# Kernel optimization log

Hardware: AMD Instinct MI355X
Metric: run time of the kernel (lower is better)

## Reference

```python
import jax, jax.numpy as jnp
import numpy as np

MAX_SET_SIZE = 32  # f1_query_max_set_size


def setup_inputs() -> dict:
    key = jax.random.key(0)
    k1, k2, k3, k4 = jax.random.split(key, 4)
    B, Lq, L, d_qk, d_v = 8, 512, 4096, 64, 64
    q = jax.random.normal(k1, (B, Lq, d_qk), dtype=jnp.float32)
    k = jax.random.normal(k2, (B, L, d_qk), dtype=jnp.float32)
    v = jax.random.normal(k3, (B, L, d_v), dtype=jnp.float32)
    mask = jax.random.randint(k4, (B * Lq, L), 0, 2).astype(bool)
    return {"q": q, "k": k, "v": v, "mask": mask}


def _query_conditioned_subset_pool(rank_scores, v, batch_idx, mask, max_set_size):
    # rank_scores/mask: [N, L]; v: [B, L, d_v]
    N, L = rank_scores.shape
    keep = min(max_set_size, L)
    neg_inf = jnp.finfo(rank_scores.dtype).min
    masked_scores = jnp.where(mask, rank_scores.astype(jnp.float32), neg_inf)
    _, top_idx = jax.lax.top_k(masked_scores, keep)          # [N, keep]
    picked = jnp.take_along_axis(mask, top_idx, axis=1)
    sortable = jnp.where(picked, top_idx, L)                 # sentinel L for unpicked
    sortable = jnp.sort(sortable, axis=1)                    # restore index order
    picked = sortable < L
    safe_idx = jnp.where(picked, sortable, 0)                # [N, keep]
    sel_v = v[batch_idx[:, None], safe_idx]                  # [N, keep, d_v]
    sel_scores = jnp.take_along_axis(rank_scores, safe_idx, axis=1)
    sel_scores = jnp.where(picked, sel_scores, neg_inf)
    attn = jax.nn.softmax(sel_scores, axis=1)
    non_empty = picked.any(axis=1, keepdims=True)
    attn = jnp.where(picked & non_empty, attn, jnp.zeros_like(attn))
    return jnp.einsum('nk,nkd->nd', attn.astype(sel_v.dtype), sel_v)


def reference(q, k, v, mask):
    B, Lq, d_qk = q.shape
    L = k.shape[1]
    d_v = v.shape[-1]
    scale = 1.0 / float(np.sqrt(d_qk))
    # rank_scores [B, Lq, L] -> flat chains [B*Lq, L]
    rank_scores = jnp.einsum('bqd,bld->bql', q, k) * scale
    rs_flat = rank_scores.reshape(B * Lq, L)
    batch_idx = jnp.repeat(jnp.arange(B), Lq)
    # f1 = mean over masked support: sum_v / clamp(count, 1)
    mask_f = mask.astype(q.dtype)                            # [B*Lq, L]
    count = jnp.clip(mask_f.sum(axis=1), 1.0, None)          # [B*Lq]
    sum_v = jnp.einsum('bql,bld->bqd', mask_f.reshape(B, Lq, L), v).reshape(B * Lq, d_v)
    mean_out = sum_v / count[:, None]
    # f1_query_mode='add': query-conditioned restricted pooling over top-k subset
    q_ctx = _query_conditioned_subset_pool(rs_flat, v, batch_idx, mask, MAX_SET_SIZE)
    out = mean_out + q_ctx
    return out.reshape(B, Lq, d_v)
```

## Files before the change

### kernel.cpp

```cpp
#include <hip/hip_runtime.h>
#include <float.h>
#include <math.h>

#define LQ   512
#define LL   4096
#define DD   64
#define KEEP 32
#define NB   8
#define NROWS (NB * LQ)

#define RT    32
#define NLC   8
#define LC    (LL / NLC)
#define LSP   128
#define NPAIR (LC / LSP)

#define WS_CI    (NROWS * NLC * KEEP)
#define WS_VT    (2 * NROWS * NLC * KEEP)
#define WS_TOTAL (WS_VT + (NB * DD * LL) / 2)

#define MASKED_KEY 0x00800000u

typedef short  bf16x8 __attribute__((ext_vector_type(8)));
typedef float  f32x4  __attribute__((ext_vector_type(4)));

__device__ __forceinline__ float dot4(float4 a, float4 b) {
    return a.x * b.x + a.y * b.y + a.z * b.z + a.w * b.w;
}
__device__ __forceinline__ unsigned short f2bf(float f) {
    unsigned int u = __float_as_uint(f);
    return (unsigned short)((u + 0x7FFFu + ((u >> 16) & 1u)) >> 16);
}
__device__ __forceinline__ unsigned int f2key(float f) {
    unsigned int u = __float_as_uint(f);
    return ((int)u < 0) ? ~u : (u | 0x80000000u);
}

#define TP_LB 256
__global__ __launch_bounds__(256) void k_vt(
    const float* __restrict__ v, unsigned short* __restrict__ vt)
{
    __shared__ unsigned short tile[DD][TP_LB + 8];
    const int t  = threadIdx.x;
    const int b  = blockIdx.x >> 4;
    const int l0 = (blockIdx.x & 15) * TP_LB;

    const float4* vg = reinterpret_cast<const float4*>(v + ((size_t)b * LL + l0) * DD);
    #pragma unroll
    for (int i = 0; i < 16; ++i) {
        int j = t + 256 * i;
        float4 f = vg[j];
        int l = j >> 4, dq = (j & 15) * 4;
        tile[dq + 0][l] = f2bf(f.x);
        tile[dq + 1][l] = f2bf(f.y);
        tile[dq + 2][l] = f2bf(f.z);
        tile[dq + 3][l] = f2bf(f.w);
    }
    __syncthreads();
    const int d = t >> 2, seg = t & 3;
    const uint4* src = reinterpret_cast<const uint4*>(&tile[d][seg * 64]);
    uint4* dst = reinterpret_cast<uint4*>(vt + ((size_t)b * DD + d) * LL + l0 + seg * 64);
    #pragma unroll
    for (int i = 0; i < 8; ++i) dst[i] = src[i];
}

__global__ __launch_bounds__(256) void k_mean(
    const int* __restrict__ mask,
    const unsigned short* __restrict__ vt,
    float* __restrict__ out)
{
    __shared__ float sums[4][4][16][16];
    __shared__ float cnt_s[4][16];

    const int t     = threadIdx.x;
    const int wave  = t >> 6;
    const int lane  = t & 63;
    const int n0    = blockIdx.x * 16;
    const int b     = n0 / LQ;
    const int row_a = lane & 15;
    const int chunk = lane >> 4;

    const int* mrow = mask + (size_t)(n0 + row_a) * LL + wave * 1024 + chunk * 8;
    const unsigned short* vbase = vt + (size_t)b * DD * LL + wave * 1024 + chunk * 8;

    f32x4 acc[4];
    #pragma unroll
    for (int dt = 0; dt < 4; ++dt) acc[dt] = (f32x4){0.f, 0.f, 0.f, 0.f};
    int cnt = 0;

    for (int l0 = 0; l0 < 1024; l0 += 32) {
        int4 ma = *reinterpret_cast<const int4*>(mrow + l0);
        int4 mb = *reinterpret_cast<const int4*>(mrow + l0 + 4);
        cnt += (ma.x != 0) + (ma.y != 0) + (ma.z != 0) + (ma.w != 0)
             + (mb.x != 0) + (mb.y != 0) + (mb.z != 0) + (mb.w != 0);
        unsigned int p[4];
        p[0] = (ma.x ? 0x3F80u : 0u) | (ma.y ? 0x3F800000u : 0u);
        p[1] = (ma.z ? 0x3F80u : 0u) | (ma.w ? 0x3F800000u : 0u);
        p[2] = (mb.x ? 0x3F80u : 0u) | (mb.y ? 0x3F800000u : 0u);
        p[3] = (mb.z ? 0x3F80u : 0u) | (mb.w ? 0x3F800000u : 0u);
        bf16x8 afrag = *reinterpret_cast<bf16x8*>(p);
        #pragma unroll
        for (int dt = 0; dt < 4; ++dt) {
            bf16x8 bfrag = *reinterpret_cast<const bf16x8*>(
                vbase + (size_t)(dt * 16 + row_a) * LL + l0);
            acc[dt] = __builtin_amdgcn_mfma_f32_16x16x32_bf16(afrag, bfrag, acc[dt], 0, 0, 0);
        }
    }
    cnt += __shfl_xor(cnt, 16);
    cnt += __shfl_xor(cnt, 32);
    if (lane < 16) cnt_s[wave][lane] = (float)cnt;
    #pragma unroll
    for (int dt = 0; dt < 4; ++dt)
        #pragma unroll
        for (int r = 0; r < 4; ++r)
            sums[wave][dt][chunk * 4 + r][row_a] = acc[dt][r];
    __syncthreads();

    const int d = t & 63, rgrp = t >> 6;
    #pragma unroll
    for (int rr = 0; rr < 4; ++rr) {
        const int row = rgrp * 4 + rr;
        float s = sums[0][d >> 4][row][d & 15] + sums[1][d >> 4][row][d & 15]
                + sums[2][d >> 4][row][d & 15] + sums[3][d >> 4][row][d & 15];
        float c = cnt_s[0][row] + cnt_s[1][row] + cnt_s[2][row] + cnt_s[3][row];
        if (c < 1.f) c = 1.f;
        out[(size_t)(n0 + row) * DD + d] = s / c;
    }
}

__global__ __launch_bounds__(256)
__attribute__((amdgpu_waves_per_eu(2, 4)))
void k_scores(
    const float* __restrict__ q,
    const float* __restrict__ kmat,
    const int*   __restrict__ mask,
    unsigned int* __restrict__ ck,
    int*          __restrict__ ci)
{
    __shared__ float4 Ss4[16 * LSP];

    const int t    = threadIdx.x;
    const int wave = t >> 6;
    const int lane = t & 63;
    const int rt   = blockIdx.x >> 3;
    const int lc   = blockIdx.x & (NLC - 1);
    const int n0   = rt * RT;
    const int b    = n0 / LQ;
    const int lbase = lc * LC;

    int qbase[8];
    #pragma unroll
    for (int p = 0; p < 8; ++p)
        qbase[p] = __builtin_amdgcn_readfirstlane((n0 + wave * 8 + p) * DD);

    const float4* kg = reinterpret_cast<const float4*>(kmat) + (size_t)b * LL * 16;

    unsigned int key[8][2 * NPAIR];

    #pragma unroll
    for (int s = 0; s < NPAIR; ++s) {
        const int l0 = lbase + s * LSP;
        __syncthreads();
        #pragma unroll
        for (int i = 0; i < 2; ++i)
            #pragma unroll
            for (int j = 0; j < 4; ++j)
                Ss4[(wave * 4 + j) * LSP + lane + 64 * i] =
                    kg[(size_t)(l0 + lane + 64 * i) * 16 + wave * 4 + j];
        __syncthreads();

        float acc0[8], acc1[8];
        #pragma unroll
        for (int p = 0; p < 8; ++p) { acc0[p] = 0.f; acc1[p] = 0.f; }
        #pragma unroll
        for (int dc = 0; dc < 16; ++dc) {
            float4 ka = Ss4[dc * LSP + lane];
            float4 kb = Ss4[dc * LSP + 64 + lane];
            #pragma unroll
            for (int p = 0; p < 8; ++p) {
                float4 q4 = *reinterpret_cast<const float4*>(q + qbase[p] + dc * 4);
                acc0[p] += dot4(ka, q4);
                acc1[p] += dot4(kb, q4);
            }
        }
        #pragma unroll
        for (int p = 0; p < 8; ++p) {
            const int r = wave * 8 + p;
            int m0 = mask[(size_t)(n0 + r) * LL + l0 + lane];
            int m1 = mask[(size_t)(n0 + r) * LL + l0 + 64 + lane];
            key[p][2 * s]     = m0 ? f2key(acc0[p] * 0.125f) : MASKED_KEY;
            key[p][2 * s + 1] = m1 ? f2key(acc1[p] * 0.125f) : MASKED_KEY;
        }
    }

    const unsigned long long lmask =
        (lane == 63) ? 0x7fffffffffffffffull : ((1ull << lane) - 1ull);
    #pragma unroll
    for (int p = 0; p < 8; ++p) {
        const int row = n0 + wave * 8 + p;
        unsigned int T = 0u;
        for (int bit = 31; bit >= 0; --bit) {
            const unsigned int cand = T | (1u << bit);
            int cnt = 0;
            #pragma unroll
            for (int e = 0; e < 2 * NPAIR; ++e)
                cnt += (int)__popcll(__ballot(key[p][e] >= cand));
            if (cnt >= KEEP) T = cand;
        }
        const bool take_eq = (T != MASKED_KEY);
        unsigned int* ckr = ck + ((size_t)row * NLC + lc) * KEEP;
        int*          cir = ci + ((size_t)row * NLC + lc) * KEEP;
        int nsel = 0;
        #pragma unroll
        for (int e = 0; e < 2 * NPAIR; ++e) {
            unsigned long long bg = __ballot(key[p][e] > T);
            int pre = (int)__popcll(bg & lmask);
            if (key[p][e] > T) {
                ckr[nsel + pre] = key[p][e];
                cir[nsel + pre] = lbase + ((e >> 1) << 7) + ((e & 1) << 6) + lane;
            }
            nsel += (int)__popcll(bg);
        }
        if (take_eq) {
            int rem = KEEP - nsel;
            #pragma unroll
            for (int e = 0; e < 2 * NPAIR; ++e) {
                if (rem <= 0) break;
                unsigned long long be = __ballot(key[p][e] == T);
                int pre = (int)__popcll(be & lmask);
                if (key[p][e] == T && pre < rem) {
                    ckr[nsel + pre] = T;
                    cir[nsel + pre] = lbase + ((e >> 1) << 7) + ((e & 1) << 6) + lane;
                }
                int c = (int)__popcll(be); if (c > rem) c = rem;
                nsel += c; rem -= c;
            }
        }
        if (lane >= nsel && lane < KEEP) { ckr[lane] = MASKED_KEY; cir[lane] = 0; }
    }
}

__global__ __launch_bounds__(256) void k_select(
    const float* __restrict__ vmat,
    const unsigned int* __restrict__ ck,
    const int* __restrict__ ci,
    float*       __restrict__ out)
{
    __shared__ unsigned int selKey[4][KEEP];
    __shared__ int          selIdx[4][KEEP];
    __shared__ float        wsel[4][KEEP];
    __shared__ int          selCnt[4], eqCnt[4];

    const int t    = threadIdx.x;
    const int wave = t >> 6;
    const int lane = t & 63;
    const int row  = blockIdx.x * 4 + wave;
    const int b    = row / LQ;

    float o = out[(size_t)row * DD + lane];

    uint4 kk = reinterpret_cast<const uint4*>(ck + (size_t)row * (NLC * KEEP))[lane];
    int4  ii = reinterpret_cast<const int4*>(ci + (size_t)row * (NLC * KEEP))[lane];
    unsigned int key[4] = { kk.x, kk.y, kk.z, kk.w };
    int          idx[4] = { ii.x, ii.y, ii.z, ii.w };

    unsigned int T = 0u;
    for (int bit = 31; bit >= 0; --bit) {
        const unsigned int cand = T | (1u << bit);
        int cnt = 0;
        #pragma unroll
        for (int e = 0; e < 4; ++e)
            cnt += (int)__popcll(__ballot(key[e] >= cand));
        if (cnt >= KEEP) T = cand;
    }
    int cgt = 0;
    #pragma unroll
    for (int e = 0; e < 4; ++e)
        cgt += (int)__popcll(__ballot(key[e] > T));
    const unsigned int quota = (unsigned int)(KEEP - cgt);
    const bool take_eq = (T != MASKED_KEY);

    if (lane < KEEP) { wsel[wave][lane] = 0.f; selIdx[wave][lane] = 0; }
    if (lane == 0)   { selCnt[wave] = 0; eqCnt[wave] = 0; }
    __asm__ volatile("s_waitcnt lgkmcnt(0)" ::: "memory");
    #pragma unroll
    for (int e = 0; e < 4; ++e) {
        unsigned int k = key[e];
        if (k > T) {
            int slot = atomicAdd(&selCnt[wave], 1);
            selKey[wave][slot] = k;
            selIdx[wave][slot] = idx[e];
        } else if (take_eq && k == T) {
            int t2 = atomicAdd(&eqCnt[wave], 1);
            if (t2 < (int)quota) {
                int slot = atomicAdd(&selCnt[wave], 1);
                selKey[wave][slot] = k;
                selIdx[wave][slot] = idx[e];
            }
        }
    }
    __asm__ volatile("s_waitcnt lgkmcnt(0)" ::: "memory");
    const int S = selCnt[wave];

    if (S > 0) {
        float vj = -FLT_MAX;
        if (lane < S) {
            unsigned int kk2 = selKey[wave][lane];
            unsigned int u = (kk2 & 0x80000000u) ? (kk2 ^ 0x80000000u) : ~kk2;
            vj = __uint_as_float(u);
        }
        float mx = vj;
        #pragma unroll
        for (int off = 1; off < 64; off <<= 1) mx = fmaxf(mx, __shfl_xor(mx, off));
        float e = (lane < S) ? expf(vj - mx) : 0.f;
        float sum = e;
        #pragma unroll
        for (int off = 1; off < 64; off <<= 1) sum += __shfl_xor(sum, off);
        if (lane < S) wsel[wave][lane] = e / sum;
        __asm__ volatile("s_waitcnt lgkmcnt(0)" ::: "memory");
        const float* vb = vmat + (size_t)b * LL * DD + lane;
        #pragma unroll
        for (int j = 0; j < KEEP; ++j) {
            float wj = wsel[wave][j];
            int   ij = selIdx[wave][j];
            o += wj * vb[(size_t)ij * DD];
        }
    }
    out[(size_t)row * DD + lane] = o;
}

#define QT   2
#define NT   256
#define NTILES (LL / NT)

__global__ __launch_bounds__(NT, 4) void ga_fused_fb(
    const float* __restrict__ q, const float* __restrict__ kmat,
    const float* __restrict__ vmat, const int* __restrict__ mask,
    float* __restrict__ out)
{
    __shared__ float sc[QT][LL];
    __shared__ float q_s[QT][DD];
    __shared__ unsigned long long mbits[QT][LL / 64];
    __shared__ float redv[4][QT][DD];
    __shared__ float mean_s[QT][DD];
    __shared__ int   count_s[QT];
    __shared__ int   sel_idx[QT][KEEP];
    __shared__ float sel_val[QT][KEEP];
    __shared__ int   sel_cnt[QT];
    __shared__ float wred[4];
    __shared__ int   ired[4];
    __shared__ int   brk;
    __shared__ float wgt[QT][KEEP];

    const int t = threadIdx.x, wave = t >> 6, lane = t & 63;
    const int n0 = blockIdx.x * QT, b = n0 / LQ;

    if (t < QT) sel_cnt[t] = 0;
    if (t < QT * DD) q_s[t >> 6][t & 63] = q[(size_t)(n0 + (t >> 6)) * DD + (t & 63)];
    __syncthreads();

    const float4* q4_0 = reinterpret_cast<const float4*>(&q_s[0][0]);
    const float4* q4_1 = reinterpret_cast<const float4*>(&q_s[1][0]);
    for (int tile = 0; tile < NTILES; ++tile) {
        int l = tile * NT + t;
        const float4* kr = reinterpret_cast<const float4*>(kmat + (size_t)(b * LL + l) * DD);
        float d0 = 0.f, d1 = 0.f;
        #pragma unroll
        for (int i = 0; i < 16; ++i) {
            float4 kk = kr[i], qa = q4_0[i], qb = q4_1[i];
            d0 += kk.x * qa.x + kk.y * qa.y + kk.z * qa.z + kk.w * qa.w;
            d1 += kk.x * qb.x + kk.y * qb.y + kk.z * qb.z + kk.w * qb.w;
        }
        int mv0 = mask[(size_t)n0 * LL + l];
        int mv1 = mask[(size_t)(n0 + 1) * LL + l];
        unsigned long long b0 = __ballot(mv0 != 0);
        unsigned long long b1 = __ballot(mv1 != 0);
        if (lane == 0) { mbits[0][tile * 4 + wave] = b0; mbits[1][tile * 4 + wave] = b1; }
        sc[0][l] = mv0 ? d0 * 0.125f : -FLT_MAX;
        sc[1][l] = mv1 ? d1 * 0.125f : -FLT_MAX;
    }
    __syncthreads();

    if (wave < QT) {
        int c = (int)__popcll(mbits[wave][lane]);
        for (int off = 32; off >= 1; off >>= 1) c += __shfl_down(c, off);
        if (lane == 0) count_s[wave] = c;
    }
    {
        float acc0 = 0.f, acc1 = 0.f;
        const int g = wave, d = lane;
        for (int wi = 0; wi < LL / 64; ++wi) {
            unsigned long long w0 = mbits[0][wi], w1 = mbits[1][wi];
            const float* vp = vmat + (size_t)(b * LL + wi * 64 + g) * DD + d;
            #pragma unroll 4
            for (int ii = 0; ii < 16; ++ii) {
                int sh = g + 4 * ii;
                float vv = vp[(size_t)(4 * ii) * DD];
                if ((w0 >> sh) & 1ULL) acc0 += vv;
                if ((w1 >> sh) & 1ULL) acc1 += vv;
            }
        }
        redv[g][0][d] = acc0; redv[g][1][d] = acc1;
    }
    __syncthreads();
    if (t < QT * DD) {
        int qt = t >> 6, dd = t & 63;
        float s2 = redv[0][qt][dd] + redv[1][qt][dd] + redv[2][qt][dd] + redv[3][qt][dd];
        int c = count_s[qt]; if (c < 1) c = 1;
        mean_s[qt][dd] = s2 / (float)c;
    }
    __syncthreads();

    for (int qt = 0; qt < QT; ++qt) {
        for (int s = 0; s < KEEP; ++s) {
            float m = -FLT_MAX; int mi = LL;
            for (int j = 0; j < NTILES; ++j) {
                int l = j * NT + t;
                float val = sc[qt][l];
                if (val > m) { m = val; mi = l; }
            }
            for (int off = 32; off >= 1; off >>= 1) {
                float ov = __shfl_down(m, off);
                int   oi = __shfl_down(mi, off);
                if (ov > m || (ov == m && oi < mi)) { m = ov; mi = oi; }
            }
            if (lane == 0) { wred[wave] = m; ired[wave] = mi; }
            __syncthreads();
            if (t == 0) {
                float bv = wred[0]; int bi = ired[0];
                for (int w2 = 1; w2 < 4; ++w2) {
                    float ov = wred[w2]; int oi = ired[w2];
                    if (ov > bv || (ov == bv && oi < bi)) { bv = ov; bi = oi; }
                }
                if (bv > -FLT_MAX) {
                    sel_idx[qt][s] = bi; sel_val[qt][s] = bv; sel_cnt[qt] = s + 1;
                    sc[qt][bi] = -FLT_MAX; brk = 0;
                } else brk = 1;
            }
            __syncthreads();
            if (brk) break;
        }
    }

    if (wave < QT) {
        int qt = wave, S = sel_cnt[qt];
        if (S > 0) {
            float mx = sel_val[qt][0];
            float e = 0.f;
            if (lane < S) e = expf(sel_val[qt][lane] - mx);
            float ssum = e;
            for (int off = 32; off >= 1; off >>= 1) ssum += __shfl_xor(ssum, off);
            if (lane < S) wgt[qt][lane] = e / ssum;
        }
    }
    __syncthreads();
    if (wave < QT) {
        int qt = wave, S = sel_cnt[qt];
        float o = mean_s[qt][lane];
        for (int j = 0; j < S; ++j)
            o += wgt[qt][j] * vmat[(size_t)(b * LL + sel_idx[qt][j]) * DD + lane];
        out[(size_t)(n0 + qt) * DD + lane] = o;
    }
}

extern "C" void kernel_launch(void* const* d_in, const int* in_sizes, int n_in,
                              void* d_out, int out_size, void* d_ws, size_t ws_size,
                              hipStream_t stream) {
    const float* q    = (const float*)d_in[0];
    const float* kmat = (const float*)d_in[1];
    const float* vmat = (const float*)d_in[2];
    const int*   mask = (const int*)d_in[3];
    float* out = (float*)d_out;

    const size_t need = (size_t)WS_TOTAL * sizeof(float);
    if (ws_size >= need) {
        float* ws = (float*)d_ws;
        unsigned int* ck = (unsigned int*)ws;
        int*          ci = (int*)(ws + WS_CI);
        unsigned short* vt = (unsigned short*)(ws + WS_VT);
        hipLaunchKernelGGL(k_scores, dim3((NROWS / RT) * NLC), dim3(256), 0, stream,
                           q, kmat, mask, ck, ci);
        hipLaunchKernelGGL(k_vt, dim3(NB * 16), dim3(256), 0, stream, vmat, vt);
        hipLaunchKernelGGL(k_mean, dim3(NROWS / 16), dim3(256), 0, stream,
                           mask, vt, out);
        hipLaunchKernelGGL(k_select, dim3(NROWS / 4), dim3(256), 0, stream,
                           vmat, ck, ci, out);
    } else {
        hipLaunchKernelGGL(ga_fused_fb, dim3(NROWS / QT), dim3(NT), 0, stream,
                           q, kmat, vmat, mask, out);
    }
}
```

Baseline: 303.3 us.

## Pack int mask into bitmask once and share it across scores and mean kernels

Adds a packing kernel that turns the 4-byte-per-element mask into 32-bit bit words in workspace. Both k_scores and k_mean then read the compact bitmask instead of the full int mask, so the 64MB mask is read once rather than twice. k_mean moves to 512 threads with 8 waves splitting L, and the top-k threshold search in k_scores interleaves the 8 rows per bit to expose more independent work. The cost is an extra kernel launch and a serial dependency on the pack pass.

```diff
diff --git a/kernel.cpp b/kernel.cpp
--- a/kernel.cpp
+++ b/kernel.cpp
@@ -8,6 +8,7 @@
 #define KEEP 32
 #define NB   8
 #define NROWS (NB * LQ)
+#define LW   (LL / 32)
 
 #define RT    32
 #define NLC   8
@@ -17,7 +18,8 @@
 
 #define WS_CI    (NROWS * NLC * KEEP)
 #define WS_VT    (2 * NROWS * NLC * KEEP)
-#define WS_TOTAL (WS_VT + (NB * DD * LL) / 2)
+#define WS_PM    (WS_VT + (NB * DD * LL) / 2)
+#define WS_TOTAL (WS_PM + NROWS * LW)
 
 #define MASKED_KEY 0x00800000u
 
@@ -34,6 +36,23 @@
 __device__ __forceinline__ unsigned int f2key(float f) {
     unsigned int u = __float_as_uint(f);
     return ((int)u < 0) ? ~u : (u | 0x80000000u);
+}
+
+__global__ __launch_bounds__(256) void k_pack(
+    const int* __restrict__ mask, unsigned int* __restrict__ pm)
+{
+    __shared__ unsigned int wbuf[4][64];
+    const int t = threadIdx.x, wave = t >> 6, lane = t & 63;
+    const size_t gw = (size_t)blockIdx.x * 4 + wave;
+    const int* src = mask + gw * 2048;
+    #pragma unroll
+    for (int i = 0; i < 32; ++i) {
+        unsigned long long b = __ballot(src[i * 64 + lane] != 0);
+        if (lane == 0) wbuf[wave][2 * i]     = (unsigned int)b;
+        if (lane == 1) wbuf[wave][2 * i + 1] = (unsigned int)(b >> 32);
+    }
+    __asm__ volatile("s_waitcnt lgkmcnt(0)" ::: "memory");
+    pm[gw * 64 + lane] = wbuf[wave][lane];
 }
 
 #define TP_LB 256
@@ -64,13 +83,13 @@
     for (int i = 0; i < 8; ++i) dst[i] = src[i];
 }
 
-__global__ __launch_bounds__(256) void k_mean(
-    const int* __restrict__ mask,
+__global__ __launch_bounds__(512) void k_mean(
+    const unsigned int* __restrict__ pm,
     const unsigned short* __restrict__ vt,
     float* __restrict__ out)
 {
-    __shared__ float sums[4][4][16][16];
-    __shared__ float cnt_s[4][16];
+    __shared__ float sums[8][4][16][16];
+    __shared__ float cnt_s[8][16];
 
     const int t     = threadIdx.x;
     const int wave  = t >> 6;
@@ -80,25 +99,26 @@
     const int row_a = lane & 15;
     const int chunk = lane >> 4;
 
-    const int* mrow = mask + (size_t)(n0 + row_a) * LL + wave * 1024 + chunk * 8;
-    const unsigned short* vbase = vt + (size_t)b * DD * LL + wave * 1024 + chunk * 8;
+    const unsigned int* prow = pm + (size_t)(n0 + row_a) * LW + wave * 16;
+    const unsigned short* vbase = vt + (size_t)b * DD * LL + wave * 512 + chunk * 8;
 
     f32x4 acc[4];
     #pragma unroll
     for (int dt = 0; dt < 4; ++dt) acc[dt] = (f32x4){0.f, 0.f, 0.f, 0.f};
     int cnt = 0;
 
-    for (int l0 = 0; l0 < 1024; l0 += 32) {
-        int4 ma = *reinterpret_cast<const int4*>(mrow + l0);
-        int4 mb = *reinterpret_cast<const int4*>(mrow + l0 + 4);
-        cnt += (ma.x != 0) + (ma.y != 0) + (ma.z != 0) + (ma.w != 0)
-             + (mb.x != 0) + (mb.y != 0) + (mb.z != 0) + (mb.w != 0);
+    #pragma unroll
+    for (int it = 0; it < 16; ++it) {
+        const unsigned int wbits = prow[it];
+        const unsigned int byte  = (wbits >> (chunk * 8)) & 0xFFu;
+        cnt += __popc(byte);
         unsigned int p[4];
-        p[0] = (ma.x ? 0x3F80u : 0u) | (ma.y ? 0x3F800000u : 0u);
-        p[1] = (ma.z ? 0x3F80u : 0u) | (ma.w ? 0x3F800000u : 0u);
-        p[2] = (mb.x ? 0x3F80u : 0u) | (mb.y ? 0x3F800000u : 0u);
-        p[3] = (mb.z ? 0x3F80u : 0u) | (mb.w ? 0x3F800000u : 0u);
+        p[0] = ((byte & 1u)   ? 0x3F80u : 0u) | ((byte & 2u)   ? 0x3F800000u : 0u);
+        p[1] = ((byte & 4u)   ? 0x3F80u : 0u) | ((byte & 8u)   ? 0x3F800000u : 0u);
+        p[2] = ((byte & 16u)  ? 0x3F80u : 0u) | ((byte & 32u)  ? 0x3F800000u : 0u);
+        p[3] = ((byte & 64u)  ? 0x3F80u : 0u) | ((byte & 128u) ? 0x3F800000u : 0u);
         bf16x8 afrag = *reinterpret_cast<bf16x8*>(p);
+        const int l0 = it * 32;
         #pragma unroll
         for (int dt = 0; dt < 4; ++dt) {
             bf16x8 bfrag = *reinterpret_cast<const bf16x8*>(
@@ -118,11 +138,14 @@
 
     const int d = t & 63, rgrp = t >> 6;
     #pragma unroll
-    for (int rr = 0; rr < 4; ++rr) {
-        const int row = rgrp * 4 + rr;
-        float s = sums[0][d >> 4][row][d & 15] + sums[1][d >> 4][row][d & 15]
-                + sums[2][d >> 4][row][d & 15] + sums[3][d >> 4][row][d & 15];
-        float c = cnt_s[0][row] + cnt_s[1][row] + cnt_s[2][row] + cnt_s[3][row];
+    for (int rr = 0; rr < 2; ++rr) {
+        const int row = rgrp * 2 + rr;
+        float s = 0.f, c = 0.f;
+        #pragma unroll
+        for (int w = 0; w < 8; ++w) {
+            s += sums[w][d >> 4][row][d & 15];
+            c += cnt_s[w][row];
+        }
         if (c < 1.f) c = 1.f;
         out[(size_t)(n0 + row) * DD + d] = s / c;
     }
@@ -133,7 +156,7 @@
 void k_scores(
     const float* __restrict__ q,
     const float* __restrict__ kmat,
-    const int*   __restrict__ mask,
+    const unsigned int* __restrict__ pm,
     unsigned int* __restrict__ ck,
     int*          __restrict__ ci)
 {
@@ -185,37 +208,47 @@
         }
         #pragma unroll
         for (int p = 0; p < 8; ++p) {
-            const int r = wave * 8 + p;
-            int m0 = mask[(size_t)(n0 + r) * LL + l0 + lane];
-            int m1 = mask[(size_t)(n0 + r) * LL + l0 + 64 + lane];
+            const int r = n0 + wave * 8 + p;
+            const unsigned int* prow = pm + (size_t)r * LW;
+            unsigned int w0 = prow[(l0 >> 5) + (lane >> 5)];
+            unsigned int w1 = prow[(l0 >> 5) + 2 + (lane >> 5)];
+            int m0 = (w0 >> (lane & 31)) & 1;
+            int m1 = (w1 >> (lane & 31)) & 1;
             key[p][2 * s]     = m0 ? f2key(acc0[p] * 0.125f) : MASKED_KEY;
             key[p][2 * s + 1] = m1 ? f2key(acc1[p] * 0.125f) : MASKED_KEY;
         }
     }
 
-    const unsigned long long lmask =
-        (lane == 63) ? 0x7fffffffffffffffull : ((1ull << lane) - 1ull);
-    #pragma unroll
-    for (int p = 0; p < 8; ++p) {
-        const int row = n0 + wave * 8 + p;
-        unsigned int T = 0u;
-        for (int bit = 31; bit >= 0; --bit) {
-            const unsigned int cand = T | (1u << bit);
+    unsigned int T[8];
+    #pragma unroll
+    for (int p = 0; p < 8; ++p) T[p] = 0u;
+    for (int bit = 31; bit >= 0; --bit) {
+        #pragma unroll
+        for (int p = 0; p < 8; ++p) {
+            const unsigned int cand = T[p] | (1u << bit);
             int cnt = 0;
             #pragma unroll
             for (int e = 0; e < 2 * NPAIR; ++e)
                 cnt += (int)__popcll(__ballot(key[p][e] >= cand));
-            if (cnt >= KEEP) T = cand;
-        }
-        const bool take_eq = (T != MASKED_KEY);
+            if (cnt >= KEEP) T[p] = cand;
+        }
+    }
+
+    const unsigned long long lmask =
+        (lane == 63) ? 0x7fffffffffffffffull : ((1ull << lane) - 1ull);
+    #pragma unroll
+    for (int p = 0; p < 8; ++p) {
+        const int row = n0 + wave * 8 + p;
+        const unsigned int Tp = T[p];
+        const bool take_eq = (Tp != MASKED_KEY);
         unsigned int* ckr = ck + ((size_t)row * NLC + lc) * KEEP;
         int*          cir = ci + ((size_t)row * NLC + lc) * KEEP;
         int nsel = 0;
         #pragma unroll
         for (int e = 0; e < 2 * NPAIR; ++e) {
-            unsigned long long bg = __ballot(key[p][e] > T);
+            unsigned long long bg = __ballot(key[p][e] > Tp);
             int pre = (int)__popcll(bg & lmask);
-            if (key[p][e] > T) {
+            if (key[p][e] > Tp) {
                 ckr[nsel + pre] = key[p][e];
                 cir[nsel + pre] = lbase + ((e >> 1) << 7) + ((e & 1) << 6) + lane;
             }
@@ -226,10 +259,10 @@
             #pragma unroll
             for (int e = 0; e < 2 * NPAIR; ++e) {
                 if (rem <= 0) break;
-                unsigned long long be = __ballot(key[p][e] == T);
+                unsigned long long be = __ballot(key[p][e] == Tp);
                 int pre = (int)__popcll(be & lmask);
-                if (key[p][e] == T && pre < rem) {
-                    ckr[nsel + pre] = T;
+                if (key[p][e] == Tp && pre < rem) {
+                    ckr[nsel + pre] = Tp;
                     cir[nsel + pre] = lbase + ((e >> 1) << 7) + ((e & 1) << 6) + lane;
                 }
                 int c = (int)__popcll(be); if (c > rem) c = rem;
@@ -478,11 +511,14 @@
         unsigned int* ck = (unsigned int*)ws;
         int*          ci = (int*)(ws + WS_CI);
         unsigned short* vt = (unsigned short*)(ws + WS_VT);
+        unsigned int* pm = (unsigned int*)(ws + WS_PM);
+        hipLaunchKernelGGL(k_pack, dim3(NROWS * LL / (2048 * 4)), dim3(256), 0, stream,
+                           mask, pm);
+        hipLaunchKernelGGL(k_vt, dim3(NB * 16), dim3(256), 0, stream, vmat, vt);
         hipLaunchKernelGGL(k_scores, dim3((NROWS / RT) * NLC), dim3(256), 0, stream,
-                           q, kmat, mask, ck, ci);
-        hipLaunchKernelGGL(k_vt, dim3(NB * 16), dim3(256), 0, stream, vmat, vt);
-        hipLaunchKernelGGL(k_mean, dim3(NROWS / 16), dim3(256), 0, stream,
-                           mask, vt, out);
+                           q, kmat, pm, ck, ci);
+        hipLaunchKernelGGL(k_mean, dim3(NROWS / 16), dim3(512), 0, stream,
+                           pm, vt, out);
         hipLaunchKernelGGL(k_select, dim3(NROWS / 4), dim3(256), 0, stream,
                            vmat, ck, ci, out);
     } else {
```

Result: slower. 427.1 us (+40.8%).
